# Kernel tuning notes

Hardware: AMD Instinct MI355X
Metric: run time of the kernel (lower is better)

## Reference

```python
import jax, jax.numpy as jnp
import numpy as np

DIM = 256
HID = 512  # max(dim, hidden_dim)
N_SLOTS = 8
ITERS = 3
EPS = 1e-8
LN_EPS = 1e-5  # torch LayerNorm default
SCALE = DIM ** -0.5


def _ln(x, g, b):
    m = jnp.mean(x, axis=-1, keepdims=True)
    v = jnp.mean(jnp.square(x - m), axis=-1, keepdims=True)
    return (x - m) * jax.lax.rsqrt(v + LN_EPS) * g + b


def setup_inputs() -> dict:
    key = jax.random.key(0)
    ks = jax.random.split(key, 16)
    s = lambda fan_in: 1.0 / np.sqrt(fan_in)
    inp = {
        "inputs": jax.random.normal(ks[0], (64, 4096, DIM), jnp.float32),
        "slots_init": jax.random.normal(ks[1], (64, N_SLOTS, DIM), jnp.float32),
        "slots_mu": jax.random.normal(ks[2], (1, 1, DIM), jnp.float32),
        "slots_sigma": jax.random.normal(ks[3], (1, 1, DIM), jnp.float32),
        "wq": jax.random.uniform(ks[4], (DIM, DIM), jnp.float32, -s(DIM), s(DIM)),
        "bq": jnp.zeros((DIM,), jnp.float32),
        "wk": jax.random.uniform(ks[5], (DIM, DIM), jnp.float32, -s(DIM), s(DIM)),
        "bk": jnp.zeros((DIM,), jnp.float32),
        "wv": jax.random.uniform(ks[6], (DIM, DIM), jnp.float32, -s(DIM), s(DIM)),
        "bv": jnp.zeros((DIM,), jnp.float32),
        "w_ih": jax.random.uniform(ks[7], (3 * DIM, DIM), jnp.float32, -s(DIM), s(DIM)),
        "b_ih": jax.random.uniform(ks[8], (3 * DIM,), jnp.float32, -s(DIM), s(DIM)),
        "w_hh": jax.random.uniform(ks[9], (3 * DIM, DIM), jnp.float32, -s(DIM), s(DIM)),
        "b_hh": jax.random.uniform(ks[10], (3 * DIM,), jnp.float32, -s(DIM), s(DIM)),
        "mlp_w1": jax.random.uniform(ks[11], (HID, DIM), jnp.float32, -s(DIM), s(DIM)),
        "mlp_b1": jnp.zeros((HID,), jnp.float32),
        "mlp_w2": jax.random.uniform(ks[12], (DIM, HID), jnp.float32, -s(HID), s(HID)),
        "mlp_b2": jnp.zeros((DIM,), jnp.float32),
        "ln_in_g": jnp.ones((DIM,), jnp.float32),
        "ln_in_b": jnp.zeros((DIM,), jnp.float32),
        "ln_slots_g": jnp.ones((DIM,), jnp.float32),
        "ln_slots_b": jnp.zeros((DIM,), jnp.float32),
        "ln_ff_g": jnp.ones((DIM,), jnp.float32),
        "ln_ff_b": jnp.zeros((DIM,), jnp.float32),
    }
    return inp


def _gru_cell(x, h, w_ih, b_ih, w_hh, b_hh):
    # torch.nn.GRUCell: gates ordered (r, z, n)
    gi = x @ w_ih.T + b_ih  # [b, s, 3d]
    gh = h @ w_hh.T + b_hh
    i_r, i_z, i_n = jnp.split(gi, 3, axis=-1)
    h_r, h_z, h_n = jnp.split(gh, 3, axis=-1)
    r = jax.nn.sigmoid(i_r + h_r)
    z = jax.nn.sigmoid(i_z + h_z)
    n = jnp.tanh(i_n + r * h_n)
    return (1.0 - z) * n + z * h


def reference(inputs, slots_init, slots_mu, slots_sigma, wq, bq, wk, bk, wv, bv,
              w_ih, b_ih, w_hh, b_hh, mlp_w1, mlp_b1, mlp_w2, mlp_b2,
              ln_in_g, ln_in_b, ln_slots_g, ln_slots_b, ln_ff_g, ln_ff_b):
    x = _ln(inputs, ln_in_g, ln_in_b)           # [b, n, d]
    k = x @ wk.T + bk
    v = x @ wv.T + bv
    slots = slots_mu + slots_sigma * slots_init  # [b, s, d]
    for _ in range(ITERS):
        slots_prev = slots
        q = _ln(slots, ln_slots_g, ln_slots_b) @ wq.T + bq
        dots = jnp.einsum('bid,bjd->bij', q, k) * SCALE  # [b, s, n]
        attn = jax.nn.softmax(dots, axis=1) + EPS        # softmax over slots
        attn = attn / jnp.sum(attn, axis=-1, keepdims=True)
        updates = jnp.einsum('bij,bjd->bid', attn, v)    # [b, s, d]
        slots = _gru_cell(updates, slots_prev, w_ih, b_ih, w_hh, b_hh)
        h = jax.nn.relu(_ln(slots, ln_ff_g, ln_ff_b) @ mlp_w1.T + mlp_b1)
        slots = slots + (h @ mlp_w2.T + mlp_b2)
    return slots
```

## Files before the change

### kernel.cpp

```cpp
#include <hip/hip_runtime.h>
#include <hip/hip_bf16.h>

#define B_ 64
#define N_ 4096
#define D_ 256
#define S_ 8
#define HID_ 512
#define NCH_ 16

typedef __attribute__((ext_vector_type(8))) short short8;
typedef __attribute__((ext_vector_type(4))) float f32x4;

__device__ inline unsigned int f2bf(float f){
  unsigned int x = __builtin_bit_cast(unsigned int, f);
  unsigned int r = x + 0x7fffu + ((x >> 16) & 1u);
  return (r >> 16);
}
__device__ inline float bf2f(unsigned int u){
  unsigned int x = (u & 0xffffu) << 16;
  return __builtin_bit_cast(float, x);
}

__global__ __launch_bounds__(256) void kLN(const float* __restrict__ xin,
    const float* __restrict__ lng, const float* __restrict__ lnb,
    unsigned short* __restrict__ xh)
{
  const int t = threadIdx.x;
  const int wv = t >> 6, lane = t & 63;
  const float4 g4 = *(const float4*)(lng + lane * 4);
  const float4 b4 = *(const float4*)(lnb + lane * 4);
#pragma unroll 2
  for (int it = 0; it < 32; ++it){
    const long r = (long)it * 8192 + blockIdx.x * 4 + wv;
    float4 f = *(const float4*)(xin + r * 256 + lane * 4);
    float s  = f.x + f.y + f.z + f.w;
    float ss = f.x*f.x + f.y*f.y + f.z*f.z + f.w*f.w;
#pragma unroll
    for (int o = 1; o < 64; o <<= 1){ s += __shfl_xor(s, o); ss += __shfl_xor(ss, o); }
    const float mean = s * (1.f/256.f);
    const float rstd = rsqrtf(ss * (1.f/256.f) - mean * mean + 1e-5f);
    unsigned p0 = f2bf((f.x - mean)*rstd*g4.x + b4.x) | (f2bf((f.y - mean)*rstd*g4.y + b4.y) << 16);
    unsigned p1 = f2bf((f.z - mean)*rstd*g4.z + b4.z) | (f2bf((f.w - mean)*rstd*g4.w + b4.w) << 16);
    uint2 pk; pk.x = p0; pk.y = p1;
    *(uint2*)(xh + r * 256 + lane * 4) = pk;
  }
}

__global__ __launch_bounds__(256) void kPre(
    const float* __restrict__ wq, const float* __restrict__ bq,
    const float* __restrict__ wk, const float* __restrict__ bk,
    const float* __restrict__ wv, const float* __restrict__ bv,
    const float* __restrict__ wih, const float* __restrict__ bih,
    float* __restrict__ Mb, float* __restrict__ cb,
    float* __restrict__ v1b, float* __restrict__ c0b,
    float* __restrict__ Wih2, float* __restrict__ bih2)
{
  const int blk = blockIdx.x, t = threadIdx.x;
  if (blk < 256){
    const int d = blk;
    float acc = 0.f, accc = 0.f;
    for (int e = 0; e < 256; ++e){
      float wkd = wk[e*256 + d];
      acc  += wkd * wq[e*256 + t];
      accc += wkd * bq[e];
    }
    Mb[d*256 + t] = acc;
    if (t == 0) cb[d] = accc;
  } else if (blk < 1024){
    const int g = blk - 256;
    float acc = 0.f, accb = 0.f;
    for (int d = 0; d < 256; ++d){
      float wg = wih[g*256 + d];
      acc  += wg * wv[d*256 + t];
      accb += wg * bv[d];
    }
    Wih2[g*256 + t] = acc;
    if (t == 0) bih2[g] = bih[g] + accb;
  } else {
    float acc = 0.f, acc0 = 0.f;
    for (int e = 0; e < 256; ++e){
      float bke = bk[e];
      acc  += wq[e*256 + t] * bke;
      acc0 += bq[e] * bke;
    }
    v1b[t] = acc;
    if (t == 0) c0b[0] = acc0;
  }
}

__global__ __launch_bounds__(256) void kI(const float* __restrict__ init,
    const float* __restrict__ mu, const float* __restrict__ sig,
    const float* __restrict__ lsg, const float* __restrict__ lsb,
    const float* __restrict__ Mb, const float* __restrict__ cb,
    const float* __restrict__ v1b, const float* __restrict__ c0b,
    float* __restrict__ slots, float* __restrict__ qt, float* __restrict__ dbuf)
{
  const int b = blockIdx.x, t = threadIdx.x;
  __shared__ float xs[S_ * D_];
  __shared__ float red[4 * S_ * 2];
  __shared__ float redd[4 * S_];
  float sv[S_];
  const float muv = mu[t], sgv = sig[t];
#pragma unroll
  for (int i = 0; i < S_; ++i){
    float x = muv + sgv * init[(b*S_ + i)*D_ + t];
    sv[i] = x;
    slots[(b*S_ + i)*D_ + t] = x;
  }
  float s[S_], qq[S_];
#pragma unroll
  for (int i = 0; i < S_; ++i){ s[i] = sv[i]; qq[i] = sv[i]*sv[i]; }
#pragma unroll
  for (int o = 1; o < 64; o <<= 1){
#pragma unroll
    for (int i = 0; i < S_; ++i){ s[i] += __shfl_xor(s[i], o); qq[i] += __shfl_xor(qq[i], o); }
  }
  const int wv_ = t >> 6;
  if ((t & 63) == 0){
#pragma unroll
    for (int i = 0; i < S_; ++i){ red[(wv_*S_ + i)*2] = s[i]; red[(wv_*S_ + i)*2 + 1] = qq[i]; }
  }
  __syncthreads();
  const float g_ = lsg[t], bv_ = lsb[t];
#pragma unroll
  for (int i = 0; i < S_; ++i){
    float S0 = 0.f, Q0 = 0.f;
#pragma unroll
    for (int w2 = 0; w2 < 4; ++w2){ S0 += red[(w2*S_ + i)*2]; Q0 += red[(w2*S_ + i)*2 + 1]; }
    float mean = S0 * (1.f/256.f), var = Q0 * (1.f/256.f) - mean*mean;
    float rstd = rsqrtf(var + 1e-5f);
    xs[i*D_ + t] = (sv[i] - mean) * rstd * g_ + bv_;
  }
  __syncthreads();
  {
    const float v1v = v1b[t];
    float pd[S_];
#pragma unroll
    for (int i = 0; i < S_; ++i) pd[i] = xs[i*D_ + t] * v1v;
#pragma unroll
    for (int o = 1; o < 64; o <<= 1)
#pragma unroll
      for (int i = 0; i < S_; ++i) pd[i] += __shfl_xor(pd[i], o);
    if ((t & 63) == 0){
#pragma unroll
      for (int i = 0; i < S_; ++i) redd[wv_*S_ + i] = pd[i];
    }
    __syncthreads();
    if (t < S_) dbuf[b*S_ + t] = redd[t] + redd[S_ + t] + redd[2*S_ + t] + redd[3*S_ + t] + c0b[0];
  }
  const float4* wr = (const float4*)(Mb + (long)t * D_);
  float acc[S_];
#pragma unroll
  for (int i = 0; i < S_; ++i) acc[i] = 0.f;
  for (int kc = 0; kc < 64; ++kc){
    float4 wf = wr[kc];
#pragma unroll
    for (int i = 0; i < S_; ++i){
      float4 xf = *(const float4*)(xs + i*D_ + kc*4);
      acc[i] += wf.x*xf.x + wf.y*xf.y + wf.z*xf.z + wf.w*xf.w;
    }
  }
  const float cbv = cb[t];
#pragma unroll
  for (int i = 0; i < S_; ++i) qt[(b*S_ + i)*D_ + t] = acc[i] + cbv;
}

__global__ __launch_bounds__(256) void kD(const unsigned short* __restrict__ xh,
    const float* __restrict__ qt, const float* __restrict__ dbuf,
    float* __restrict__ numP, float* __restrict__ denP)
{
  const int b = blockIdx.y, ch = blockIdx.x, t = threadIdx.x;
  __shared__ __align__(16) unsigned short qs[16 * 264];
  __shared__ float sw[S_ * 132];
  const int lane = t & 63, w = t >> 6;
  const int lr = lane & 15, lg = lane >> 4;
  const int i_ = t >> 5, oct = t & 31;

  {
    const int rowq = t >> 4, segq = t & 15;
    uint4 z0 = {0,0,0,0}, z1 = {0,0,0,0};
    if (rowq < 8){
      const float* qr = qt + ((long)b * S_ + rowq) * D_ + segq * 16;
      float4 f0 = ((const float4*)qr)[0], f1 = ((const float4*)qr)[1];
      float4 f2 = ((const float4*)qr)[2], f3 = ((const float4*)qr)[3];
      z0.x = f2bf(f0.x)|(f2bf(f0.y)<<16); z0.y = f2bf(f0.z)|(f2bf(f0.w)<<16);
      z0.z = f2bf(f1.x)|(f2bf(f1.y)<<16); z0.w = f2bf(f1.z)|(f2bf(f1.w)<<16);
      z1.x = f2bf(f2.x)|(f2bf(f2.y)<<16); z1.y = f2bf(f2.z)|(f2bf(f2.w)<<16);
      z1.z = f2bf(f3.x)|(f2bf(f3.y)<<16); z1.w = f2bf(f3.z)|(f2bf(f3.w)<<16);
    }
    *(uint4*)(qs + rowq*264 + segq*16) = z0;
    *(uint4*)(qs + rowq*264 + segq*16 + 8) = z1;
  }
  __syncthreads();

  short8 bqf[8];
#pragma unroll
  for (int ks = 0; ks < 8; ++ks)
    bqf[ks] = *(const short8*)(qs + lr*264 + ks*32 + lg*8);

  const float dd = (lr < 8) ? dbuf[b*S_ + lr] * 0.0625f : 0.f;

  float acc[8] = {0,0,0,0,0,0,0,0};
  float denl = 0.f;

  auto ACC = [&](uint4 v, float wg){
    acc[0] += wg * bf2f(v.x); acc[1] += wg * bf2f(v.x >> 16);
    acc[2] += wg * bf2f(v.y); acc[3] += wg * bf2f(v.y >> 16);
    acc[4] += wg * bf2f(v.z); acc[5] += wg * bf2f(v.z >> 16);
    acc[6] += wg * bf2f(v.w); acc[7] += wg * bf2f(v.w >> 16);
  };

  for (int ph = 0; ph < 2; ++ph){
    const long j0 = (long)ch * 256 + ph * 128;
#pragma unroll
    for (int tau = 0; tau < 2; ++tau){
      const long jt = j0 + w*32 + tau*16;
      const unsigned short* kr = xh + ((long)b * N_ + jt + lr) * 256;
      f32x4 d = {0,0,0,0};
#pragma unroll
      for (int ks = 0; ks < 8; ++ks){
        short8 afk = *(const short8*)(kr + ks*32 + lg*8);
        d = __builtin_amdgcn_mfma_f32_16x16x32_bf16(afk, bqf[ks], d, 0, 0, 0);
      }
#pragma unroll
      for (int r = 0; r < 4; ++r){
        float x = d[r] * 0.0625f + dd;
        float m = x;
        m = fmaxf(m, __shfl_xor(m, 1));
        m = fmaxf(m, __shfl_xor(m, 2));
        m = fmaxf(m, __shfl_xor(m, 4));
        float e = __expf(x - m);
        float ssum = e;
        ssum += __shfl_xor(ssum, 1);
        ssum += __shfl_xor(ssum, 2);
        ssum += __shfl_xor(ssum, 4);
        float wv = e / ssum + 1e-8f;
        if (lr < 8) sw[lr*132 + w*32 + tau*16 + lg*4 + r] = wv;
      }
    }
    __syncthreads();
    const unsigned short* vrow = xh + ((long)b * N_ + j0) * 256 + oct*8;
    const float* swr = sw + i_ * 132;
    uint4 va0, va1, va2, va3, vb0, vb1, vb2, vb3;
    {
      const unsigned short* p0 = vrow;
      va0 = *(const uint4*)(p0);       va1 = *(const uint4*)(p0 + 256);
      va2 = *(const uint4*)(p0 + 512); va3 = *(const uint4*)(p0 + 768);
    }
    for (int g = 0; g < 16; ++g){
      const unsigned short* pb = vrow + (long)(g*8 + 4) * 256;
      vb0 = *(const uint4*)(pb);       vb1 = *(const uint4*)(pb + 256);
      vb2 = *(const uint4*)(pb + 512); vb3 = *(const uint4*)(pb + 768);
      float4 w4 = *(const float4*)(swr + g*8);
      ACC(va0, w4.x); ACC(va1, w4.y); ACC(va2, w4.z); ACC(va3, w4.w);
      denl += w4.x + w4.y + w4.z + w4.w;
      if (g < 15){
        const unsigned short* pa = vrow + (long)(g*8 + 8) * 256;
        va0 = *(const uint4*)(pa);       va1 = *(const uint4*)(pa + 256);
        va2 = *(const uint4*)(pa + 512); va3 = *(const uint4*)(pa + 768);
      }
      float4 w5 = *(const float4*)(swr + g*8 + 4);
      ACC(vb0, w5.x); ACC(vb1, w5.y); ACC(vb2, w5.z); ACC(vb3, w5.w);
      denl += w5.x + w5.y + w5.z + w5.w;
    }
    __syncthreads();
  }

  float* numC = numP + ((((long)ch * B_ + b) * S_ + i_) * D_) + oct * 8;
  float4 a0 = {acc[0], acc[1], acc[2], acc[3]};
  float4 a1 = {acc[4], acc[5], acc[6], acc[7]};
  *(float4*)(numC) = a0;
  *(float4*)(numC + 4) = a1;
  if (oct == 0) denP[((long)b * S_ + i_) * NCH_ + ch] = denl;
}

__device__ inline void stats2(const float v[2], float* red, int t, float* mean, float* rstd){
  float s[2], q2[2];
#pragma unroll
  for (int ii = 0; ii < 2; ++ii){ s[ii] = v[ii]; q2[ii] = v[ii]*v[ii]; }
#pragma unroll
  for (int o = 1; o < 64; o <<= 1){
#pragma unroll
    for (int ii = 0; ii < 2; ++ii){ s[ii] += __shfl_xor(s[ii], o); q2[ii] += __shfl_xor(q2[ii], o); }
  }
  const int wv = t >> 6;
  if ((t & 63) == 0){
#pragma unroll
    for (int ii = 0; ii < 2; ++ii){ red[(wv*2 + ii)*2] = s[ii]; red[(wv*2 + ii)*2 + 1] = q2[ii]; }
  }
  __syncthreads();
#pragma unroll
  for (int ii = 0; ii < 2; ++ii){
    float S0 = 0.f, Q0 = 0.f;
#pragma unroll
    for (int w2 = 0; w2 < 4; ++w2){ S0 += red[(w2*2 + ii)*2]; Q0 += red[(w2*2 + ii)*2 + 1]; }
    float m = S0 * (1.f/256.f);
    float var = Q0 * (1.f/256.f) - m*m;
    mean[ii] = m; rstd[ii] = rsqrtf(var + 1e-5f);
  }
  __syncthreads();
}

__global__ __launch_bounds__(256) void kS(
    const float* __restrict__ numP, const float* __restrict__ denP,
    const float* __restrict__ slots_in,
    const float* __restrict__ Wih2, const float* __restrict__ bih2,
    const float* __restrict__ w_hh, const float* __restrict__ b_hh,
    const float* __restrict__ w1, const float* __restrict__ b1,
    const float* __restrict__ w2, const float* __restrict__ b2,
    const float* __restrict__ fg, const float* __restrict__ fb,
    const float* __restrict__ lsg, const float* __restrict__ lsb,
    const float* __restrict__ Mb, const float* __restrict__ cbv,
    const float* __restrict__ v1b, const float* __restrict__ c0b,
    float* __restrict__ outp, float* __restrict__ qout, float* __restrict__ dbuf,
    int write_q)
{
  const int blk = blockIdx.x;
  const int b = blk >> 2, i0 = (blk & 3) * 2;
  const int t = threadIdx.x;
  const int grp = t >> 3, j = t & 7;
  __shared__ float us[2][D_], hs[2][D_], xs2[2][D_];
  __shared__ float gi_l[2][768], gh_l[2][768];
  __shared__ float h2s[2][HID_];
  __shared__ float o2[2][D_];
  __shared__ float red[4 * 2 * 2];
  const long base = (long)(b * S_ + i0) * D_;
#pragma unroll
  for (int ii = 0; ii < 2; ++ii){
    int si = b*S_ + i0 + ii;
    float dv = 0.f;
#pragma unroll
    for (int ch = 0; ch < NCH_; ++ch) dv += denP[(long)si * NCH_ + ch];
    float u = 0.f;
    for (int ch = 0; ch < NCH_; ++ch)
      u += numP[(((long)ch * B_ + b) * S_ + i0 + ii) * D_ + t];
    us[ii][t] = u / dv;
    hs[ii][t] = slots_in[base + ii*D_ + t];
  }
  __syncthreads();
  for (int q = 0; q < 24; ++q){
    const int gcol = grp + q * 32;
    const float4* wi = (const float4*)(Wih2 + (long)gcol * D_) + j;
    const float4* wh = (const float4*)(w_hh + (long)gcol * D_) + j;
    float ai[2] = {0,0}, ah[2] = {0,0};
#pragma unroll
    for (int c = 0; c < 8; ++c){
      float4 wf = wi[c*8];
      float4 hf = wh[c*8];
      const int k4 = (j + c*8) * 4;
#pragma unroll
      for (int ii = 0; ii < 2; ++ii){
        float4 uf = *(const float4*)(&us[ii][k4]);
        float4 hv = *(const float4*)(&hs[ii][k4]);
        ai[ii] += wf.x*uf.x + wf.y*uf.y + wf.z*uf.z + wf.w*uf.w;
        ah[ii] += hf.x*hv.x + hf.y*hv.y + hf.z*hv.z + hf.w*hv.w;
      }
    }
#pragma unroll
    for (int o = 1; o < 8; o <<= 1){
#pragma unroll
      for (int ii = 0; ii < 2; ++ii){ ai[ii] += __shfl_xor(ai[ii], o); ah[ii] += __shfl_xor(ah[ii], o); }
    }
    if (j == 0){
#pragma unroll
      for (int ii = 0; ii < 2; ++ii){ gi_l[ii][gcol] = ai[ii]; gh_l[ii][gcol] = ah[ii]; }
    }
  }
  __syncthreads();
  const float bir = bih2[t], biz = bih2[256 + t], bin_ = bih2[512 + t];
  const float bhr = b_hh[t], bhz = b_hh[256 + t], bhn = b_hh[512 + t];
  float nh[2];
#pragma unroll
  for (int ii = 0; ii < 2; ++ii){
    float r = 1.f / (1.f + __expf(-(gi_l[ii][t] + bir + gh_l[ii][t] + bhr)));
    float z = 1.f / (1.f + __expf(-(gi_l[ii][256 + t] + biz + gh_l[ii][256 + t] + bhz)));
    float n = tanhf(gi_l[ii][512 + t] + bin_ + r * (gh_l[ii][512 + t] + bhn));
    nh[ii] = (1.f - z) * n + z * hs[ii][t];
  }
  float mean[2], rstd[2];
  stats2(nh, red, t, mean, rstd);
  const float fgv = fg[t], fbv = fb[t];
#pragma unroll
  for (int ii = 0; ii < 2; ++ii) xs2[ii][t] = (nh[ii] - mean[ii]) * rstd[ii] * fgv + fbv;
  __syncthreads();
  for (int q = 0; q < 16; ++q){
    const int gcol = grp + q * 32;
    const float4* wr = (const float4*)(w1 + (long)gcol * D_) + j;
    float a[2] = {0,0};
#pragma unroll
    for (int c = 0; c < 8; ++c){
      float4 wf = wr[c*8];
      const int k4 = (j + c*8) * 4;
#pragma unroll
      for (int ii = 0; ii < 2; ++ii){
        float4 xf = *(const float4*)(&xs2[ii][k4]);
        a[ii] += wf.x*xf.x + wf.y*xf.y + wf.z*xf.z + wf.w*xf.w;
      }
    }
#pragma unroll
    for (int o = 1; o < 8; o <<= 1)
#pragma unroll
      for (int ii = 0; ii < 2; ++ii) a[ii] += __shfl_xor(a[ii], o);
    if (j == 0){
      float bb = b1[gcol];
#pragma unroll
      for (int ii = 0; ii < 2; ++ii) h2s[ii][gcol] = fmaxf(a[ii] + bb, 0.f);
    }
  }
  __syncthreads();
  for (int q = 0; q < 8; ++q){
    const int gcol = grp + q * 32;
    const float4* wr = (const float4*)(w2 + (long)gcol * HID_) + j;
    float a[2] = {0,0};
#pragma unroll
    for (int c = 0; c < 16; ++c){
      float4 wf = wr[c*8];
      const int k4 = (j + c*8) * 4;
#pragma unroll
      for (int ii = 0; ii < 2; ++ii){
        float4 xf = *(const float4*)(&h2s[ii][k4]);
        a[ii] += wf.x*xf.x + wf.y*xf.y + wf.z*xf.z + wf.w*xf.w;
      }
    }
#pragma unroll
    for (int o = 1; o < 8; o <<= 1)
#pragma unroll
      for (int ii = 0; ii < 2; ++ii) a[ii] += __shfl_xor(a[ii], o);
    if (j == 0){
#pragma unroll
      for (int ii = 0; ii < 2; ++ii) o2[ii][gcol] = a[ii];
    }
  }
  __syncthreads();
  float outv[2];
  const float b2v = b2[t];
#pragma unroll
  for (int ii = 0; ii < 2; ++ii){
    outv[ii] = nh[ii] + o2[ii][t] + b2v;
    outp[base + ii*D_ + t] = outv[ii];
  }
  if (write_q){
    float mean2[2], rstd2[2];
    stats2(outv, red, t, mean2, rstd2);
    const float lg2 = lsg[t], lb2 = lsb[t];
#pragma unroll
    for (int ii = 0; ii < 2; ++ii) xs2[ii][t] = (outv[ii] - mean2[ii]) * rstd2[ii] * lg2 + lb2;
    __syncthreads();
    {
      const float v1v = v1b[t];
      float pd[2];
#pragma unroll
      for (int ii = 0; ii < 2; ++ii) pd[ii] = xs2[ii][t] * v1v;
#pragma unroll
      for (int o = 1; o < 64; o <<= 1)
#pragma unroll
        for (int ii = 0; ii < 2; ++ii) pd[ii] += __shfl_xor(pd[ii], o);
      const int wv = t >> 6;
      if ((t & 63) == 0){ red[wv*2] = pd[0]; red[wv*2 + 1] = pd[1]; }
      __syncthreads();
      if (t < 2) dbuf[b*S_ + i0 + t] = red[t] + red[2 + t] + red[4 + t] + red[6 + t] + c0b[0];
    }
    for (int q = 0; q < 8; ++q){
      const int gcol = grp + q * 32;
      const float4* wr = (const float4*)(Mb + (long)gcol * D_) + j;
      float a[2] = {0,0};
#pragma unroll
      for (int c = 0; c < 8; ++c){
        float4 wf = wr[c*8];
        const int k4 = (j + c*8) * 4;
#pragma unroll
        for (int ii = 0; ii < 2; ++ii){
          float4 xf = *(const float4*)(&xs2[ii][k4]);
          a[ii] += wf.x*xf.x + wf.y*xf.y + wf.z*xf.z + wf.w*xf.w;
        }
      }
#pragma unroll
      for (int o = 1; o < 8; o <<= 1)
#pragma unroll
        for (int ii = 0; ii < 2; ++ii) a[ii] += __shfl_xor(a[ii], o);
      if (j == 0){
        float bb = cbv[gcol];
#pragma unroll
        for (int ii = 0; ii < 2; ++ii) qout[(long)(b*S_ + i0 + ii)*D_ + gcol] = a[ii] + bb;
      }
    }
  }
}

extern "C" void kernel_launch(void* const* d_in, const int* in_sizes, int n_in,
                              void* d_out, int out_size, void* d_ws, size_t ws_size,
                              hipStream_t stream)
{
  const float* inputs     = (const float*)d_in[0];
  const float* slots_init = (const float*)d_in[1];
  const float* slots_mu   = (const float*)d_in[2];
  const float* slots_sig  = (const float*)d_in[3];
  const float* wq   = (const float*)d_in[4];
  const float* bq   = (const float*)d_in[5];
  const float* wk   = (const float*)d_in[6];
  const float* bk   = (const float*)d_in[7];
  const float* wv   = (const float*)d_in[8];
  const float* bv   = (const float*)d_in[9];
  const float* w_ih = (const float*)d_in[10];
  const float* b_ih = (const float*)d_in[11];
  const float* w_hh = (const float*)d_in[12];
  const float* b_hh = (const float*)d_in[13];
  const float* w1   = (const float*)d_in[14];
  const float* b1   = (const float*)d_in[15];
  const float* w2   = (const float*)d_in[16];
  const float* b2   = (const float*)d_in[17];
  const float* lig  = (const float*)d_in[18];
  const float* lib  = (const float*)d_in[19];
  const float* lsg  = (const float*)d_in[20];
  const float* lsb  = (const float*)d_in[21];
  const float* ffg  = (const float*)d_in[22];
  const float* ffb  = (const float*)d_in[23];
  float* out = (float*)d_out;

  char* ws = (char*)d_ws;
  float* qtb  = (float*)(ws);
  float* numP = (float*)(ws + 524288);
  float* denP = (float*)(ws + 8912896);
  float* dbuf = (float*)(ws + 8945664);
  float* Mb   = (float*)(ws + 8947712);
  float* cb   = (float*)(ws + 9209856);
  float* v1b  = (float*)(ws + 9210880);
  float* c0b  = (float*)(ws + 9211904);
  float* Wih2 = (float*)(ws + 9212928);
  float* bih2 = (float*)(ws + 9999360);
  unsigned short* xh = (unsigned short*)(ws + 10003456);
  float* slots = out;

  kLN<<<2048, 256, 0, stream>>>(inputs, lig, lib, xh);
  kPre<<<1025, 256, 0, stream>>>(wq, bq, wk, bk, wv, bv, w_ih, b_ih,
                                 Mb, cb, v1b, c0b, Wih2, bih2);
  kI<<<64, 256, 0, stream>>>(slots_init, slots_mu, slots_sig, lsg, lsb,
                             Mb, cb, v1b, c0b, slots, qtb, dbuf);
  for (int it = 0; it < 3; ++it){
    kD<<<dim3(NCH_, B_), 256, 0, stream>>>(xh, qtb, dbuf, numP, denP);
    kS<<<256, 256, 0, stream>>>(numP, denP, slots, Wih2, bih2, w_hh, b_hh,
                                w1, b1, w2, b2, ffg, ffb, lsg, lsb,
                                Mb, cb, v1b, c0b,
                                slots, qtb, dbuf, (it < 2) ? 1 : 0);
  }
}
```

Measured before the change: 473.9 us.

## Double attention chunks and give each slot its own GRU/MLP block

The attention kernel now splits the sequence into 32 chunks of 128 tokens instead of 16 chunks of 256, doubling its grid and removing the inner two-phase loop. The slot-update kernel now handles one slot per block (512 blocks) instead of two, so more blocks run in parallel. The trade-off is twice as many partial numerators for the reduction to read, and each block of the slot-update kernel re-reading the full GRU/MLP weights with half the reuse. Workspace offsets are shifted to make room for the larger partial buffer.

```diff
diff --git a/kernel.cpp b/kernel.cpp
--- a/kernel.cpp
+++ b/kernel.cpp
@@ -6,7 +6,7 @@
 #define D_ 256
 #define S_ 8
 #define HID_ 512
-#define NCH_ 16
+#define NCH_ 32
 
 typedef __attribute__((ext_vector_type(8))) short short8;
 typedef __attribute__((ext_vector_type(4))) float f32x4;
@@ -210,60 +210,57 @@
     acc[6] += wg * bf2f(v.w); acc[7] += wg * bf2f(v.w >> 16);
   };
 
-  for (int ph = 0; ph < 2; ++ph){
-    const long j0 = (long)ch * 256 + ph * 128;
-#pragma unroll
-    for (int tau = 0; tau < 2; ++tau){
-      const long jt = j0 + w*32 + tau*16;
-      const unsigned short* kr = xh + ((long)b * N_ + jt + lr) * 256;
-      f32x4 d = {0,0,0,0};
-#pragma unroll
-      for (int ks = 0; ks < 8; ++ks){
-        short8 afk = *(const short8*)(kr + ks*32 + lg*8);
-        d = __builtin_amdgcn_mfma_f32_16x16x32_bf16(afk, bqf[ks], d, 0, 0, 0);
-      }
-#pragma unroll
-      for (int r = 0; r < 4; ++r){
-        float x = d[r] * 0.0625f + dd;
-        float m = x;
-        m = fmaxf(m, __shfl_xor(m, 1));
-        m = fmaxf(m, __shfl_xor(m, 2));
-        m = fmaxf(m, __shfl_xor(m, 4));
-        float e = __expf(x - m);
-        float ssum = e;
-        ssum += __shfl_xor(ssum, 1);
-        ssum += __shfl_xor(ssum, 2);
-        ssum += __shfl_xor(ssum, 4);
-        float wv = e / ssum + 1e-8f;
-        if (lr < 8) sw[lr*132 + w*32 + tau*16 + lg*4 + r] = wv;
-      }
-    }
-    __syncthreads();
-    const unsigned short* vrow = xh + ((long)b * N_ + j0) * 256 + oct*8;
-    const float* swr = sw + i_ * 132;
-    uint4 va0, va1, va2, va3, vb0, vb1, vb2, vb3;
-    {
-      const unsigned short* p0 = vrow;
-      va0 = *(const uint4*)(p0);       va1 = *(const uint4*)(p0 + 256);
-      va2 = *(const uint4*)(p0 + 512); va3 = *(const uint4*)(p0 + 768);
-    }
-    for (int g = 0; g < 16; ++g){
-      const unsigned short* pb = vrow + (long)(g*8 + 4) * 256;
-      vb0 = *(const uint4*)(pb);       vb1 = *(const uint4*)(pb + 256);
-      vb2 = *(const uint4*)(pb + 512); vb3 = *(const uint4*)(pb + 768);
-      float4 w4 = *(const float4*)(swr + g*8);
-      ACC(va0, w4.x); ACC(va1, w4.y); ACC(va2, w4.z); ACC(va3, w4.w);
-      denl += w4.x + w4.y + w4.z + w4.w;
-      if (g < 15){
-        const unsigned short* pa = vrow + (long)(g*8 + 8) * 256;
-        va0 = *(const uint4*)(pa);       va1 = *(const uint4*)(pa + 256);
-        va2 = *(const uint4*)(pa + 512); va3 = *(const uint4*)(pa + 768);
-      }
-      float4 w5 = *(const float4*)(swr + g*8 + 4);
-      ACC(vb0, w5.x); ACC(vb1, w5.y); ACC(vb2, w5.z); ACC(vb3, w5.w);
-      denl += w5.x + w5.y + w5.z + w5.w;
-    }
-    __syncthreads();
+  const long j0 = (long)ch * 128;
+#pragma unroll
+  for (int tau = 0; tau < 2; ++tau){
+    const long jt = j0 + w*32 + tau*16;
+    const unsigned short* kr = xh + ((long)b * N_ + jt + lr) * 256;
+    f32x4 d = {0,0,0,0};
+#pragma unroll
+    for (int ks = 0; ks < 8; ++ks){
+      short8 afk = *(const short8*)(kr + ks*32 + lg*8);
+      d = __builtin_amdgcn_mfma_f32_16x16x32_bf16(afk, bqf[ks], d, 0, 0, 0);
+    }
+#pragma unroll
+    for (int r = 0; r < 4; ++r){
+      float x = d[r] * 0.0625f + dd;
+      float m = x;
+      m = fmaxf(m, __shfl_xor(m, 1));
+      m = fmaxf(m, __shfl_xor(m, 2));
+      m = fmaxf(m, __shfl_xor(m, 4));
+      float e = __expf(x - m);
+      float ssum = e;
+      ssum += __shfl_xor(ssum, 1);
+      ssum += __shfl_xor(ssum, 2);
+      ssum += __shfl_xor(ssum, 4);
+      float wv = e / ssum + 1e-8f;
+      if (lr < 8) sw[lr*132 + w*32 + tau*16 + lg*4 + r] = wv;
+    }
+  }
+  __syncthreads();
+  const unsigned short* vrow = xh + ((long)b * N_ + j0) * 256 + oct*8;
+  const float* swr = sw + i_ * 132;
+  uint4 va0, va1, va2, va3, vb0, vb1, vb2, vb3;
+  {
+    const unsigned short* p0 = vrow;
+    va0 = *(const uint4*)(p0);       va1 = *(const uint4*)(p0 + 256);
+    va2 = *(const uint4*)(p0 + 512); va3 = *(const uint4*)(p0 + 768);
+  }
+  for (int g = 0; g < 16; ++g){
+    const unsigned short* pb = vrow + (long)(g*8 + 4) * 256;
+    vb0 = *(const uint4*)(pb);       vb1 = *(const uint4*)(pb + 256);
+    vb2 = *(const uint4*)(pb + 512); vb3 = *(const uint4*)(pb + 768);
+    float4 w4 = *(const float4*)(swr + g*8);
+    ACC(va0, w4.x); ACC(va1, w4.y); ACC(va2, w4.z); ACC(va3, w4.w);
+    denl += w4.x + w4.y + w4.z + w4.w;
+    if (g < 15){
+      const unsigned short* pa = vrow + (long)(g*8 + 8) * 256;
+      va0 = *(const uint4*)(pa);       va1 = *(const uint4*)(pa + 256);
+      va2 = *(const uint4*)(pa + 512); va3 = *(const uint4*)(pa + 768);
+    }
+    float4 w5 = *(const float4*)(swr + g*8 + 4);
+    ACC(vb0, w5.x); ACC(vb1, w5.y); ACC(vb2, w5.z); ACC(vb3, w5.w);
+    denl += w5.x + w5.y + w5.z + w5.w;
   }
 
   float* numC = numP + ((((long)ch * B_ + b) * S_ + i_) * D_) + oct * 8;
@@ -274,30 +271,18 @@
   if (oct == 0) denP[((long)b * S_ + i_) * NCH_ + ch] = denl;
 }
 
-__device__ inline void stats2(const float v[2], float* red, int t, float* mean, float* rstd){
-  float s[2], q2[2];
-#pragma unroll
-  for (int ii = 0; ii < 2; ++ii){ s[ii] = v[ii]; q2[ii] = v[ii]*v[ii]; }
-#pragma unroll
-  for (int o = 1; o < 64; o <<= 1){
-#pragma unroll
-    for (int ii = 0; ii < 2; ++ii){ s[ii] += __shfl_xor(s[ii], o); q2[ii] += __shfl_xor(q2[ii], o); }
-  }
+__device__ inline void stats1(float v, float* red, int t, float* mean, float* rstd){
+  float s = v, q2 = v*v;
+#pragma unroll
+  for (int o = 1; o < 64; o <<= 1){ s += __shfl_xor(s, o); q2 += __shfl_xor(q2, o); }
   const int wv = t >> 6;
-  if ((t & 63) == 0){
-#pragma unroll
-    for (int ii = 0; ii < 2; ++ii){ red[(wv*2 + ii)*2] = s[ii]; red[(wv*2 + ii)*2 + 1] = q2[ii]; }
-  }
-  __syncthreads();
-#pragma unroll
-  for (int ii = 0; ii < 2; ++ii){
-    float S0 = 0.f, Q0 = 0.f;
-#pragma unroll
-    for (int w2 = 0; w2 < 4; ++w2){ S0 += red[(w2*2 + ii)*2]; Q0 += red[(w2*2 + ii)*2 + 1]; }
-    float m = S0 * (1.f/256.f);
-    float var = Q0 * (1.f/256.f) - m*m;
-    mean[ii] = m; rstd[ii] = rsqrtf(var + 1e-5f);
-  }
+  if ((t & 63) == 0){ red[wv*2] = s; red[wv*2 + 1] = q2; }
+  __syncthreads();
+  float S0 = red[0] + red[2] + red[4] + red[6];
+  float Q0 = red[1] + red[3] + red[5] + red[7];
+  float m = S0 * (1.f/256.f);
+  float var = Q0 * (1.f/256.f) - m*m;
+  *mean = m; *rstd = rsqrtf(var + 1e-5f);
   __syncthreads();
 }
 
@@ -316,173 +301,122 @@
     int write_q)
 {
   const int blk = blockIdx.x;
-  const int b = blk >> 2, i0 = (blk & 3) * 2;
+  const int b = blk >> 3, i0 = blk & 7;
   const int t = threadIdx.x;
   const int grp = t >> 3, j = t & 7;
-  __shared__ float us[2][D_], hs[2][D_], xs2[2][D_];
-  __shared__ float gi_l[2][768], gh_l[2][768];
-  __shared__ float h2s[2][HID_];
-  __shared__ float o2[2][D_];
-  __shared__ float red[4 * 2 * 2];
+  __shared__ float us[D_], hs[D_], xs2[D_];
+  __shared__ float gi_l[768], gh_l[768];
+  __shared__ float h2s[HID_];
+  __shared__ float o2[D_];
+  __shared__ float red[8];
   const long base = (long)(b * S_ + i0) * D_;
-#pragma unroll
-  for (int ii = 0; ii < 2; ++ii){
-    int si = b*S_ + i0 + ii;
+  {
+    const int si = b*S_ + i0;
     float dv = 0.f;
 #pragma unroll
     for (int ch = 0; ch < NCH_; ++ch) dv += denP[(long)si * NCH_ + ch];
     float u = 0.f;
     for (int ch = 0; ch < NCH_; ++ch)
-      u += numP[(((long)ch * B_ + b) * S_ + i0 + ii) * D_ + t];
-    us[ii][t] = u / dv;
-    hs[ii][t] = slots_in[base + ii*D_ + t];
+      u += numP[(((long)ch * B_ + b) * S_ + i0) * D_ + t];
+    us[t] = u / dv;
+    hs[t] = slots_in[base + t];
   }
   __syncthreads();
   for (int q = 0; q < 24; ++q){
     const int gcol = grp + q * 32;
     const float4* wi = (const float4*)(Wih2 + (long)gcol * D_) + j;
     const float4* wh = (const float4*)(w_hh + (long)gcol * D_) + j;
-    float ai[2] = {0,0}, ah[2] = {0,0};
+    float ai = 0.f, ah = 0.f;
 #pragma unroll
     for (int c = 0; c < 8; ++c){
       float4 wf = wi[c*8];
       float4 hf = wh[c*8];
       const int k4 = (j + c*8) * 4;
-#pragma unroll
-      for (int ii = 0; ii < 2; ++ii){
-        float4 uf = *(const float4*)(&us[ii][k4]);
-        float4 hv = *(const float4*)(&hs[ii][k4]);
-        ai[ii] += wf.x*uf.x + wf.y*uf.y + wf.z*uf.z + wf.w*uf.w;
-        ah[ii] += hf.x*hv.x + hf.y*hv.y + hf.z*hv.z + hf.w*hv.w;
-      }
-    }
-#pragma unroll
-    for (int o = 1; o < 8; o <<= 1){
-#pragma unroll
-      for (int ii = 0; ii < 2; ++ii){ ai[ii] += __shfl_xor(ai[ii], o); ah[ii] += __shfl_xor(ah[ii], o); }
-    }
-    if (j == 0){
-#pragma unroll
-      for (int ii = 0; ii < 2; ++ii){ gi_l[ii][gcol] = ai[ii]; gh_l[ii][gcol] = ah[ii]; }
-    }
+      float4 uf = *(const float4*)(&us[k4]);
+      float4 hv = *(const float4*)(&hs[k4]);
+      ai += wf.x*uf.x + wf.y*uf.y + wf.z*uf.z + wf.w*uf.w;
+      ah += hf.x*hv.x + hf.y*hv.y + hf.z*hv.z + hf.w*hv.w;
+    }
+#pragma unroll
+    for (int o = 1; o < 8; o <<= 1){ ai += __shfl_xor(ai, o); ah += __shfl_xor(ah, o); }
+    if (j == 0){ gi_l[gcol] = ai; gh_l[gcol] = ah; }
   }
   __syncthreads();
   const float bir = bih2[t], biz = bih2[256 + t], bin_ = bih2[512 + t];
   const float bhr = b_hh[t], bhz = b_hh[256 + t], bhn = b_hh[512 + t];
-  float nh[2];
-#pragma unroll
-  for (int ii = 0; ii < 2; ++ii){
-    float r = 1.f / (1.f + __expf(-(gi_l[ii][t] + bir + gh_l[ii][t] + bhr)));
-    float z = 1.f / (1.f + __expf(-(gi_l[ii][256 + t] + biz + gh_l[ii][256 + t] + bhz)));
-    float n = tanhf(gi_l[ii][512 + t] + bin_ + r * (gh_l[ii][512 + t] + bhn));
-    nh[ii] = (1.f - z) * n + z * hs[ii][t];
-  }
-  float mean[2], rstd[2];
-  stats2(nh, red, t, mean, rstd);
-  const float fgv = fg[t], fbv = fb[t];
-#pragma unroll
-  for (int ii = 0; ii < 2; ++ii) xs2[ii][t] = (nh[ii] - mean[ii]) * rstd[ii] * fgv + fbv;
+  float nh;
+  {
+    float r = 1.f / (1.f + __expf(-(gi_l[t] + bir + gh_l[t] + bhr)));
+    float z = 1.f / (1.f + __expf(-(gi_l[256 + t] + biz + gh_l[256 + t] + bhz)));
+    float n = tanhf(gi_l[512 + t] + bin_ + r * (gh_l[512 + t] + bhn));
+    nh = (1.f - z) * n + z * hs[t];
+  }
+  float mean, rstd;
+  stats1(nh, red, t, &mean, &rstd);
+  xs2[t] = (nh - mean) * rstd * fg[t] + fb[t];
   __syncthreads();
   for (int q = 0; q < 16; ++q){
     const int gcol = grp + q * 32;
     const float4* wr = (const float4*)(w1 + (long)gcol * D_) + j;
-    float a[2] = {0,0};
+    float a = 0.f;
 #pragma unroll
     for (int c = 0; c < 8; ++c){
       float4 wf = wr[c*8];
       const int k4 = (j + c*8) * 4;
-#pragma unroll
-      for (int ii = 0; ii < 2; ++ii){
-        float4 xf = *(const float4*)(&xs2[ii][k4]);
-        a[ii] += wf.x*xf.x + wf.y*xf.y + wf.z*xf.z + wf.w*xf.w;
-      }
-    }
-#pragma unroll
-    for (int o = 1; o < 8; o <<= 1)
-#pragma unroll
-      for (int ii = 0; ii < 2; ++ii) a[ii] += __shfl_xor(a[ii], o);
-    if (j == 0){
-      float bb = b1[gcol];
-#pragma unroll
-      for (int ii = 0; ii < 2; ++ii) h2s[ii][gcol] = fmaxf(a[ii] + bb, 0.f);
-    }
+      float4 xf = *(const float4*)(&xs2[k4]);
+      a += wf.x*xf.x + wf.y*xf.y + wf.z*xf.z + wf.w*xf.w;
+    }
+#pragma unroll
+    for (int o = 1; o < 8; o <<= 1) a += __shfl_xor(a, o);
+    if (j == 0) h2s[gcol] = fmaxf(a + b1[gcol], 0.f);
   }
   __syncthreads();
   for (int q = 0; q < 8; ++q){
     const int gcol = grp + q * 32;
     const float4* wr = (const float4*)(w2 + (long)gcol * HID_) + j;
-    float a[2] = {0,0};
+    float a = 0.f;
 #pragma unroll
     for (int c = 0; c < 16; ++c){
       float4 wf = wr[c*8];
       const int k4 = (j + c*8) * 4;
-#pragma unroll
-      for (int ii = 0; ii < 2; ++ii){
-        float4 xf = *(const float4*)(&h2s[ii][k4]);
-        a[ii] += wf.x*xf.x + wf.y*xf.y + wf.z*xf.z + wf.w*xf.w;
-      }
-    }
-#pragma unroll
-    for (int o = 1; o < 8; o <<= 1)
-#pragma unroll
-      for (int ii = 0; ii < 2; ++ii) a[ii] += __shfl_xor(a[ii], o);
-    if (j == 0){
-#pragma unroll
-      for (int ii = 0; ii < 2; ++ii) o2[ii][gcol] = a[ii];
-    }
-  }
-  __syncthreads();
-  float outv[2];
-  const float b2v = b2[t];
-#pragma unroll
-  for (int ii = 0; ii < 2; ++ii){
-    outv[ii] = nh[ii] + o2[ii][t] + b2v;
-    outp[base + ii*D_ + t] = outv[ii];
-  }
+      float4 xf = *(const float4*)(&h2s[k4]);
+      a += wf.x*xf.x + wf.y*xf.y + wf.z*xf.z + wf.w*xf.w;
+    }
+#pragma unroll
+    for (int o = 1; o < 8; o <<= 1) a += __shfl_xor(a, o);
+    if (j == 0) o2[gcol] = a;
+  }
+  __syncthreads();
+  float outv = nh + o2[t] + b2[t];
+  outp[base + t] = outv;
   if (write_q){
-    float mean2[2], rstd2[2];
-    stats2(outv, red, t, mean2, rstd2);
-    const float lg2 = lsg[t], lb2 = lsb[t];
-#pragma unroll
-    for (int ii = 0; ii < 2; ++ii) xs2[ii][t] = (outv[ii] - mean2[ii]) * rstd2[ii] * lg2 + lb2;
+    float mean2, rstd2;
+    stats1(outv, red, t, &mean2, &rstd2);
+    xs2[t] = (outv - mean2) * rstd2 * lsg[t] + lsb[t];
     __syncthreads();
     {
-      const float v1v = v1b[t];
-      float pd[2];
-#pragma unroll
-      for (int ii = 0; ii < 2; ++ii) pd[ii] = xs2[ii][t] * v1v;
-#pragma unroll
-      for (int o = 1; o < 64; o <<= 1)
-#pragma unroll
-        for (int ii = 0; ii < 2; ++ii) pd[ii] += __shfl_xor(pd[ii], o);
+      float pd = xs2[t] * v1b[t];
+#pragma unroll
+      for (int o = 1; o < 64; o <<= 1) pd += __shfl_xor(pd, o);
       const int wv = t >> 6;
-      if ((t & 63) == 0){ red[wv*2] = pd[0]; red[wv*2 + 1] = pd[1]; }
+      if ((t & 63) == 0) red[wv] = pd;
       __syncthreads();
-      if (t < 2) dbuf[b*S_ + i0 + t] = red[t] + red[2 + t] + red[4 + t] + red[6 + t] + c0b[0];
+      if (t == 0) dbuf[b*S_ + i0] = red[0] + red[1] + red[2] + red[3] + c0b[0];
     }
     for (int q = 0; q < 8; ++q){
       const int gcol = grp + q * 32;
       const float4* wr = (const float4*)(Mb + (long)gcol * D_) + j;
-      float a[2] = {0,0};
+      float a = 0.f;
 #pragma unroll
       for (int c = 0; c < 8; ++c){
         float4 wf = wr[c*8];
         const int k4 = (j + c*8) * 4;
-#pragma unroll
-        for (int ii = 0; ii < 2; ++ii){
-          float4 xf = *(const float4*)(&xs2[ii][k4]);
-          a[ii] += wf.x*xf.x + wf.y*xf.y + wf.z*xf.z + wf.w*xf.w;
-        }
+        float4 xf = *(const float4*)(&xs2[k4]);
+        a += wf.x*xf.x + wf.y*xf.y + wf.z*xf.z + wf.w*xf.w;
       }
 #pragma unroll
-      for (int o = 1; o < 8; o <<= 1)
-#pragma unroll
-        for (int ii = 0; ii < 2; ++ii) a[ii] += __shfl_xor(a[ii], o);
-      if (j == 0){
-        float bb = cbv[gcol];
-#pragma unroll
-        for (int ii = 0; ii < 2; ++ii) qout[(long)(b*S_ + i0 + ii)*D_ + gcol] = a[ii] + bb;
-      }
+      for (int o = 1; o < 8; o <<= 1) a += __shfl_xor(a, o);
+      if (j == 0) qout[(long)(b*S_ + i0)*D_ + gcol] = a + cbv[gcol];
     }
   }
 }
@@ -520,15 +454,15 @@
   char* ws = (char*)d_ws;
   float* qtb  = (float*)(ws);
   float* numP = (float*)(ws + 524288);
-  float* denP = (float*)(ws + 8912896);
-  float* dbuf = (float*)(ws + 8945664);
-  float* Mb   = (float*)(ws + 8947712);
-  float* cb   = (float*)(ws + 9209856);
-  float* v1b  = (float*)(ws + 9210880);
-  float* c0b  = (float*)(ws + 9211904);
-  float* Wih2 = (float*)(ws + 9212928);
-  float* bih2 = (float*)(ws + 9999360);
-  unsigned short* xh = (unsigned short*)(ws + 10003456);
+  float* denP = (float*)(ws + 17301504);
+  float* dbuf = (float*)(ws + 17367040);
+  float* Mb   = (float*)(ws + 17369088);
+  float* cb   = (float*)(ws + 17631232);
+  float* v1b  = (float*)(ws + 17632256);
+  float* c0b  = (float*)(ws + 17633280);
+  float* Wih2 = (float*)(ws + 17634304);
+  float* bih2 = (float*)(ws + 18420736);
+  unsigned short* xh = (unsigned short*)(ws + 18424832);
   float* slots = out;
 
   kLN<<<2048, 256, 0, stream>>>(inputs, lig, lib, xh);
@@ -538,7 +472,7 @@
                              Mb, cb, v1b, c0b, slots, qtb, dbuf);
   for (int it = 0; it < 3; ++it){
     kD<<<dim3(NCH_, B_), 256, 0, stream>>>(xh, qtb, dbuf, numP, denP);
-    kS<<<256, 256, 0, stream>>>(numP, denP, slots, Wih2, bih2, w_hh, b_hh,
+    kS<<<512, 256, 0, stream>>>(numP, denP, slots, Wih2, bih2, w_hh, b_hh,
                                 w1, b1, w2, b2, ffg, ffb, lsg, lsb,
                                 Mb, cb, v1b, c0b,
                                 slots, qtb, dbuf, (it < 2) ? 1 : 0);
```

Result: slower. 634.9 us (+34.0%).

## Restructure kD update accumulation so each wave reads only its own V rows

Applied to the files above, without the earlier changes.

Before, each thread accumulated one slot across all 128 rows of a phase, so every V row was loaded once per slot (8x redundant global reads). Now each wave handles only its own 32 rows, and each lane accumulates 4 slots for 8 features, so every V element is loaded once per block. The per-phase barrier goes away. The price is 36 accumulator registers per thread and a shared-memory cross-wave reduction at the end.

```diff
diff --git a/kernel.cpp b/kernel.cpp
--- a/kernel.cpp
+++ b/kernel.cpp
@@ -170,11 +170,13 @@
     float* __restrict__ numP, float* __restrict__ denP)
 {
   const int b = blockIdx.y, ch = blockIdx.x, t = threadIdx.x;
-  __shared__ __align__(16) unsigned short qs[16 * 264];
-  __shared__ float sw[S_ * 132];
+  __shared__ __align__(16) char smem[4 * 64 * 37 * 4];
+  __shared__ __align__(16) float sw[128 * 8];
+  unsigned short* qs = (unsigned short*)smem;
+  float* redbuf = (float*)smem;
   const int lane = t & 63, w = t >> 6;
   const int lr = lane & 15, lg = lane >> 4;
-  const int i_ = t >> 5, oct = t & 31;
+  const int oct = lane & 31, sh = lane >> 5;
 
   {
     const int rowq = t >> 4, segq = t & 15;
@@ -197,18 +199,16 @@
 #pragma unroll
   for (int ks = 0; ks < 8; ++ks)
     bqf[ks] = *(const short8*)(qs + lr*264 + ks*32 + lg*8);
+  __syncthreads();
 
   const float dd = (lr < 8) ? dbuf[b*S_ + lr] * 0.0625f : 0.f;
 
-  float acc[8] = {0,0,0,0,0,0,0,0};
-  float denl = 0.f;
-
-  auto ACC = [&](uint4 v, float wg){
-    acc[0] += wg * bf2f(v.x); acc[1] += wg * bf2f(v.x >> 16);
-    acc[2] += wg * bf2f(v.y); acc[3] += wg * bf2f(v.y >> 16);
-    acc[4] += wg * bf2f(v.z); acc[5] += wg * bf2f(v.z >> 16);
-    acc[6] += wg * bf2f(v.w); acc[7] += wg * bf2f(v.w >> 16);
-  };
+  float acc4[4][8];
+#pragma unroll
+  for (int s = 0; s < 4; ++s)
+#pragma unroll
+    for (int e = 0; e < 8; ++e) acc4[s][e] = 0.f;
+  float den4[4] = {0.f, 0.f, 0.f, 0.f};
 
   for (int ph = 0; ph < 2; ++ph){
     const long j0 = (long)ch * 256 + ph * 128;
@@ -235,43 +235,61 @@
         ssum += __shfl_xor(ssum, 2);
         ssum += __shfl_xor(ssum, 4);
         float wv = e / ssum + 1e-8f;
-        if (lr < 8) sw[lr*132 + w*32 + tau*16 + lg*4 + r] = wv;
-      }
-    }
-    __syncthreads();
-    const unsigned short* vrow = xh + ((long)b * N_ + j0) * 256 + oct*8;
-    const float* swr = sw + i_ * 132;
-    uint4 va0, va1, va2, va3, vb0, vb1, vb2, vb3;
-    {
-      const unsigned short* p0 = vrow;
-      va0 = *(const uint4*)(p0);       va1 = *(const uint4*)(p0 + 256);
-      va2 = *(const uint4*)(p0 + 512); va3 = *(const uint4*)(p0 + 768);
-    }
-    for (int g = 0; g < 16; ++g){
-      const unsigned short* pb = vrow + (long)(g*8 + 4) * 256;
-      vb0 = *(const uint4*)(pb);       vb1 = *(const uint4*)(pb + 256);
-      vb2 = *(const uint4*)(pb + 512); vb3 = *(const uint4*)(pb + 768);
-      float4 w4 = *(const float4*)(swr + g*8);
-      ACC(va0, w4.x); ACC(va1, w4.y); ACC(va2, w4.z); ACC(va3, w4.w);
-      denl += w4.x + w4.y + w4.z + w4.w;
-      if (g < 15){
-        const unsigned short* pa = vrow + (long)(g*8 + 8) * 256;
-        va0 = *(const uint4*)(pa);       va1 = *(const uint4*)(pa + 256);
-        va2 = *(const uint4*)(pa + 512); va3 = *(const uint4*)(pa + 768);
-      }
-      float4 w5 = *(const float4*)(swr + g*8 + 4);
-      ACC(vb0, w5.x); ACC(vb1, w5.y); ACC(vb2, w5.z); ACC(vb3, w5.w);
-      denl += w5.x + w5.y + w5.z + w5.w;
-    }
-    __syncthreads();
-  }
-
-  float* numC = numP + ((((long)ch * B_ + b) * S_ + i_) * D_) + oct * 8;
-  float4 a0 = {acc[0], acc[1], acc[2], acc[3]};
-  float4 a1 = {acc[4], acc[5], acc[6], acc[7]};
-  *(float4*)(numC) = a0;
-  *(float4*)(numC + 4) = a1;
-  if (oct == 0) denP[((long)b * S_ + i_) * NCH_ + ch] = denl;
+        if (lr < 8) sw[(w*32 + tau*16 + lg*4 + r)*8 + lr] = wv;
+      }
+    }
+    const unsigned short* vrow = xh + ((long)b * N_ + j0 + w*32) * 256 + oct*8;
+    const float* swr = sw + (w*32)*8 + sh*4;
+#pragma unroll 4
+    for (int j = 0; j < 32; ++j){
+      uint4 v = *(const uint4*)(vrow + (long)j * 256);
+      float4 w4 = *(const float4*)(swr + j*8);
+      float xv[8];
+      xv[0] = bf2f(v.x); xv[1] = bf2f(v.x >> 16);
+      xv[2] = bf2f(v.y); xv[3] = bf2f(v.y >> 16);
+      xv[4] = bf2f(v.z); xv[5] = bf2f(v.z >> 16);
+      xv[6] = bf2f(v.w); xv[7] = bf2f(v.w >> 16);
+#pragma unroll
+      for (int e = 0; e < 8; ++e){
+        acc4[0][e] += w4.x * xv[e];
+        acc4[1][e] += w4.y * xv[e];
+        acc4[2][e] += w4.z * xv[e];
+        acc4[3][e] += w4.w * xv[e];
+      }
+      den4[0] += w4.x; den4[1] += w4.y; den4[2] += w4.z; den4[3] += w4.w;
+    }
+  }
+
+  __syncthreads();
+  {
+    float* myred = redbuf + (w*64 + lane)*37;
+#pragma unroll
+    for (int s = 0; s < 4; ++s){
+#pragma unroll
+      for (int e = 0; e < 8; ++e) myred[s*8 + e] = acc4[s][e];
+      myred[32 + s] = den4[s];
+    }
+  }
+  __syncthreads();
+  {
+    const int i_ = t >> 5, oo = t & 31;
+    const int ssh = i_ >> 2, ss = i_ & 3;
+    float outv[8] = {0,0,0,0,0,0,0,0};
+    float den = 0.f;
+#pragma unroll
+    for (int wv2 = 0; wv2 < 4; ++wv2){
+      const float* p = redbuf + (wv2*64 + ssh*32 + oo)*37;
+#pragma unroll
+      for (int e = 0; e < 8; ++e) outv[e] += p[ss*8 + e];
+      den += p[32 + ss];
+    }
+    float* numC = numP + ((((long)ch * B_ + b) * S_ + i_) * D_) + oo * 8;
+    float4 a0 = {outv[0], outv[1], outv[2], outv[3]};
+    float4 a1 = {outv[4], outv[5], outv[6], outv[7]};
+    *(float4*)(numC) = a0;
+    *(float4*)(numC + 4) = a1;
+    if (oo == 0) denP[((long)b * S_ + i_) * NCH_ + ch] = den;
+  }
 }
 
 __device__ inline void stats2(const float v[2], float* red, int t, float* mean, float* rstd){
```

Result: faster. 420.1 us (-11.4%).
